# Optimization experiments

Hardware: AMD Instinct MI355X
Metric: run time of the kernel (lower is better)

The kernel has to match this reference:

```python
import jax, jax.numpy as jnp
import numpy as np

UNITS = 1024
D = 1024

def setup_inputs() -> dict:
    key = jax.random.key(0)
    ks = jax.random.split(key, 8)
    B, T = 32, 2048
    query = jax.random.normal(ks[0], (B, D), dtype=jnp.float32)
    values = jax.random.normal(ks[1], (B, T, D), dtype=jnp.float32)
    s1 = 1.0 / np.sqrt(D)
    s2 = 1.0 / np.sqrt(UNITS)
    W1 = jax.random.normal(ks[2], (D, UNITS), dtype=jnp.float32) * s1
    b1 = jnp.zeros((UNITS,), dtype=jnp.float32)
    W2 = jax.random.normal(ks[3], (D, UNITS), dtype=jnp.float32) * s1
    b2 = jnp.zeros((UNITS,), dtype=jnp.float32)
    Wv = jax.random.normal(ks[4], (UNITS, 1), dtype=jnp.float32) * s2
    bv = jnp.zeros((1,), dtype=jnp.float32)
    return {"query": query, "values": values, "W1": W1, "b1": b1,
            "W2": W2, "b2": b2, "Wv": Wv, "bv": bv}

def reference(query, values, W1, b1, W2, b2, Wv, bv):
    # query: [B, D]; values: [B, T, D]
    q_proj = query @ W1 + b1                     # [B, U]
    v_proj = jnp.einsum('btd,du->btu', values, W2) + b2  # [B, T, U]
    h = jnp.tanh(q_proj[:, None, :] + v_proj)    # [B, T, U]
    score = jnp.einsum('btu,uo->bto', h, Wv) + bv  # [B, T, 1]
    attention_weights = jax.nn.softmax(score, axis=1)  # [B, T, 1]
    context_vector = jnp.sum(attention_weights * values, axis=1)  # [B, D]
    return (context_vector, attention_weights)
```

## Files before the change

kernel.cpp:

```cpp
#include <hip/hip_runtime.h>
#include <hip/hip_bf16.h>
#include <stdint.h>


typedef unsigned short ushort_t;
typedef short bf16x8 __attribute__((ext_vector_type(8)));
typedef float f32x4 __attribute__((ext_vector_type(4)));

#define GLOBAL_AS __attribute__((address_space(1)))
#define LDS_AS    __attribute__((address_space(3)))

__device__ __forceinline__ ushort_t f2bf(float f) {
    union { float f; unsigned int u; } v;
    v.f = f;
    unsigned int u = v.u;
    unsigned int r = u + 0x7FFFu + ((u >> 16) & 1u);
    return (ushort_t)(r >> 16);
}
__device__ __forceinline__ unsigned int pk2(float a, float b) {
    union { __hip_bfloat162 h; unsigned int u; } c;
    c.h = __float22bfloat162_rn(make_float2(a, b));
    return c.u;
}
__device__ __forceinline__ float fast_tanh(float x) {
    float ax = __builtin_fabsf(x);
    float e = __expf(-2.0f * ax);
    float t = (1.0f - e) * __builtin_amdgcn_rcpf(1.0f + e);
    return __builtin_copysignf(t, x);
}

static constexpr int B_ = 32, T_ = 2048, D_ = 1024, U_ = 1024;
static constexpr int M_ = B_ * T_;
static constexpr int TRANS_B = 1024;
static constexpr int QPROJ_B = 512;
static constexpr int CONV_B  = 4096;

__global__ __launch_bounds__(256) void k_prep(const float* __restrict__ W2,
                                              const float* __restrict__ query,
                                              const float* __restrict__ W1,
                                              const float* __restrict__ b1,
                                              const float* __restrict__ b2,
                                              const float* __restrict__ values,
                                              ushort_t* __restrict__ W2T,
                                              float* __restrict__ qpb,
                                              ushort_t* __restrict__ vb) {
    __shared__ float smem[1280];
    int bid = blockIdx.x;
    const int tid = threadIdx.x;

    if (bid < TRANS_B) {
        float(*tile)[33] = (float(*)[33])smem;
        int u0 = (bid & 31) * 32, d0 = (bid >> 5) * 32;
        int tx = tid & 31, ty = tid >> 5;
#pragma unroll
        for (int r = 0; r < 4; ++r)
            tile[ty + r * 8][tx] = W2[(size_t)(d0 + ty + r * 8) * U_ + (u0 + tx)];
        __syncthreads();
#pragma unroll
        for (int r = 0; r < 4; ++r)
            W2T[(size_t)(u0 + ty + r * 8) * D_ + (d0 + tx)] = f2bf(tile[tx][ty + r * 8]);
        return;
    }
    bid -= TRANS_B;

    if (bid >= QPROJ_B) {
        const int cb = bid - QPROJ_B;
        const size_t base = (size_t)cb * 2048 + tid;
#pragma unroll
        for (int k = 0; k < 8; ++k) {
            const size_t chunk = base + (size_t)k * 256;
            const float* s = values + chunk * 8;
            f32x4 v0 = *(const f32x4*)s;
            f32x4 v1 = *(const f32x4*)(s + 4);
            uint4 p;
            p.x = pk2(v0[0], v0[1]);
            p.y = pk2(v0[2], v0[3]);
            p.z = pk2(v1[0], v1[1]);
            p.w = pk2(v1[2], v1[3]);
            *(uint4*)(vb + chunk * 8) = p;
        }
        return;
    }

    const int b = bid >> 4, uc = bid & 15;
    float* qs = smem;
    float* red = smem + 1024;
    for (int i = tid; i < D_; i += 256) qs[i] = query[b * D_ + i];
    __syncthreads();
    const int ul = tid & 63, ds = tid >> 6;
    const int u = uc * 64 + ul;
    float acc = 0.f;
#pragma unroll 8
    for (int d = ds * 256; d < ds * 256 + 256; ++d)
        acc += qs[d] * W1[(size_t)d * U_ + u];
    red[tid] = acc;
    __syncthreads();
    if (tid < 64) {
        int uu = uc * 64 + tid;
        qpb[b * U_ + uu] = red[tid] + red[tid + 64] + red[tid + 128] + red[tid + 192] +
                           b1[uu] + b2[uu];
    }
}

#define BM 128
#define BN 128
#define BK 64

template <bool ABF16>
__global__ __launch_bounds__(256) void k_score_gemm(const float* __restrict__ values,
                                                    const ushort_t* __restrict__ vb,
                                                    const ushort_t* __restrict__ W2T,
                                                    const float* __restrict__ qpb,
                                                    const float* __restrict__ Wv,
                                                    float* __restrict__ scores_partial) {
    __shared__ ushort_t As[BM * BK];
    __shared__ ushort_t Bs[BN * BK];
    __shared__ float sScore[BM];

    const int tid = threadIdx.x;
    const int lane = tid & 63;
    const int w = tid >> 6;
    const int wm = w >> 1, wn = w & 1;

    const int g = blockIdx.x;
    const int mt = ((g >> 6) << 3) | (g & 7);
    const int nt = (g >> 3) & 7;
    const int m0 = mt * BM, n0 = nt * BN;

    if (tid < BM) sScore[tid] = 0.f;

    f32x4 acc[4][4];
#pragma unroll
    for (int i = 0; i < 4; ++i)
#pragma unroll
        for (int j = 0; j < 4; ++j) acc[i][j] = (f32x4){0.f, 0.f, 0.f, 0.f};

    const int lr = lane >> 3;
    const int cB = (lane & 7) ^ lr;
    const ushort_t* bBase = W2T + (size_t)(n0 + w * 8 + lr) * D_ + cB * 8;
    const ushort_t* aBaseB = vb + (size_t)(m0 + w * 8 + lr) * D_ + cB * 8;

    const int rA = tid >> 3;
    const int cA = tid & 7;
    const int pA = cA ^ (rA & 7);
    const float* aSrc = values + (size_t)(m0 + rA) * D_ + cA * 8;
    ushort_t* aDst = As + rA * BK + pA * 8;

    const int quad = lane >> 4;
    const int l15 = lane & 15;
    const int l7 = l15 & 7;

    for (int k0 = 0; k0 < D_; k0 += BK) {
#pragma unroll
        for (int i = 0; i < 4; ++i) {
            __builtin_amdgcn_global_load_lds(
                (const GLOBAL_AS void*)(bBase + k0 + (size_t)i * 32 * D_),
                (LDS_AS void*)(Bs + i * 2048 + w * 512), 16, 0, 0);
        }
        if constexpr (ABF16) {
#pragma unroll
            for (int i = 0; i < 4; ++i) {
                __builtin_amdgcn_global_load_lds(
                    (const GLOBAL_AS void*)(aBaseB + k0 + (size_t)i * 32 * D_),
                    (LDS_AS void*)(As + i * 2048 + w * 512), 16, 0, 0);
            }
        } else {
#pragma unroll
            for (int i = 0; i < 4; ++i) {
                f32x4 v0 = *(const f32x4*)(aSrc + k0 + (size_t)i * 32 * D_);
                f32x4 v1 = *(const f32x4*)(aSrc + k0 + (size_t)i * 32 * D_ + 4);
                uint4 p;
                p.x = pk2(v0[0], v0[1]);
                p.y = pk2(v0[2], v0[3]);
                p.z = pk2(v1[0], v1[1]);
                p.w = pk2(v1[2], v1[3]);
                *(uint4*)(aDst + i * 32 * BK) = p;
            }
        }
        __syncthreads();
#pragma unroll
        for (int kk = 0; kk < BK; kk += 32) {
            bf16x8 af[4], bfr[4];
            const int cb = kk >> 3;
#pragma unroll
            for (int i = 0; i < 4; ++i) {
                int r = wm * 64 + i * 16 + l15;
                af[i] = *(const bf16x8*)(As + (r << 6) + (((quad + cb) ^ l7) << 3));
            }
#pragma unroll
            for (int j = 0; j < 4; ++j) {
                int r = wn * 64 + j * 16 + l15;
                bfr[j] = *(const bf16x8*)(Bs + (r << 6) + (((quad + cb) ^ l7) << 3));
            }
#pragma unroll
            for (int i = 0; i < 4; ++i)
#pragma unroll
                for (int j = 0; j < 4; ++j)
                    acc[i][j] = __builtin_amdgcn_mfma_f32_16x16x32_bf16(
                        af[i], bfr[j], acc[i][j], 0, 0, 0);
        }
        __syncthreads();
    }

    const int b = m0 >> 11;
    const float* qp = qpb + b * U_;
    float qv[4], wv[4];
#pragma unroll
    for (int j = 0; j < 4; ++j) {
        int u = n0 + wn * 64 + j * 16 + l15;
        qv[j] = qp[u];
        wv[j] = Wv[u];
    }
#pragma unroll
    for (int i = 0; i < 4; ++i) {
#pragma unroll
        for (int r = 0; r < 4; ++r) {
            float s = 0.f;
#pragma unroll
            for (int j = 0; j < 4; ++j) s += fast_tanh(acc[i][j][r] + qv[j]) * wv[j];
            s += __shfl_xor(s, 1);
            s += __shfl_xor(s, 2);
            s += __shfl_xor(s, 4);
            s += __shfl_xor(s, 8);
            if (l15 == 0) atomicAdd(&sScore[wm * 64 + i * 16 + quad * 4 + r], s);
        }
    }
    __syncthreads();
    if (tid < BM) scores_partial[(size_t)(m0 + tid) * 8 + nt] = sScore[tid];
}

__global__ __launch_bounds__(256) void k_softmax(const float* __restrict__ scores_partial,
                                                 const float* __restrict__ bv,
                                                 float* __restrict__ w_f,
                                                 float* __restrict__ out_w) {
    const int b = blockIdx.x;
    __shared__ float s[T_];
    __shared__ float red[4];
    const int tid = threadIdx.x;
    const float bvf = bv[0];

    float lmax = -1e30f;
    for (int t = tid; t < T_; t += 256) {
        const float* p = scores_partial + (size_t)(b * T_ + t) * 8;
        float sc = ((p[0] + p[1]) + (p[2] + p[3])) + ((p[4] + p[5]) + (p[6] + p[7])) + bvf;
        s[t] = sc;
        lmax = fmaxf(lmax, sc);
    }
    for (int off = 32; off; off >>= 1) lmax = fmaxf(lmax, __shfl_xor(lmax, off));
    if ((tid & 63) == 0) red[tid >> 6] = lmax;
    __syncthreads();
    const float gmax = fmaxf(fmaxf(red[0], red[1]), fmaxf(red[2], red[3]));

    float lsum = 0.f;
    for (int t = tid; t < T_; t += 256) {
        float e = __expf(s[t] - gmax);
        s[t] = e;
        lsum += e;
    }
    for (int off = 32; off; off >>= 1) lsum += __shfl_xor(lsum, off);
    __syncthreads();
    if ((tid & 63) == 0) red[tid >> 6] = lsum;
    __syncthreads();
    const float ginv = 1.f / ((red[0] + red[1]) + (red[2] + red[3]));

    for (int t = tid; t < T_; t += 256) {
        float wgt = s[t] * ginv;
        w_f[b * T_ + t] = wgt;
        out_w[b * T_ + t] = wgt;
    }
}

__global__ __launch_bounds__(256) void k_ctx(const float* __restrict__ values,
                                             const float* __restrict__ w_f,
                                             float* __restrict__ out_ctx) {
    const int tc = blockIdx.x;
    const int b = blockIdx.y;
    const int tid = threadIdx.x;
    __shared__ float wls[128];
    if (tid < 128) wls[tid] = w_f[b * T_ + tc * 128 + tid];
    __syncthreads();

    f32x4 acc = (f32x4){0.f, 0.f, 0.f, 0.f};
    const float* base = values + (size_t)(b * T_ + tc * 128) * D_ + tid * 4;
#pragma unroll 4
    for (int tt = 0; tt < 128; ++tt)
        acc += wls[tt] * *(const f32x4*)(base + (size_t)tt * D_);
    float* out = out_ctx + b * D_ + tid * 4;
    atomicAdd(&out[0], acc[0]);
    atomicAdd(&out[1], acc[1]);
    atomicAdd(&out[2], acc[2]);
    atomicAdd(&out[3], acc[3]);
}

extern "C" void kernel_launch(void* const* d_in, const int* in_sizes, int n_in,
                              void* d_out, int out_size, void* d_ws, size_t ws_size,
                              hipStream_t stream) {
    const float* query  = (const float*)d_in[0];
    const float* values = (const float*)d_in[1];
    const float* W1     = (const float*)d_in[2];
    const float* b1     = (const float*)d_in[3];
    const float* W2     = (const float*)d_in[4];
    const float* b2     = (const float*)d_in[5];
    const float* Wv     = (const float*)d_in[6];
    const float* bv     = (const float*)d_in[7];

    float* out_ctx = (float*)d_out;
    float* out_w   = out_ctx + B_ * D_;

    char* ws = (char*)d_ws;
    const size_t OFF_W2T = 0;
    const size_t OFF_QPB = 0x200000;
    const size_t OFF_SP  = 0x220000;
    const size_t OFF_WF  = 0x420000;
    const size_t OFF_VB  = 0x500000;
    const size_t VB_BYTES = (size_t)M_ * D_ * sizeof(ushort_t);

    ushort_t* W2T            = (ushort_t*)(ws + OFF_W2T);
    float*    qpb            = (float*)(ws + OFF_QPB);
    float*    scores_partial = (float*)(ws + OFF_SP);
    float*    w_f            = (float*)(ws + OFF_WF);
    ushort_t* vb             = (ushort_t*)(ws + OFF_VB);

    const bool use_bf16 = (ws_size >= OFF_VB + VB_BYTES);

    hipMemsetAsync(out_ctx, 0, (size_t)B_ * D_ * sizeof(float), stream);

    k_prep<<<dim3(TRANS_B + QPROJ_B + (use_bf16 ? CONV_B : 0)), 256, 0, stream>>>(
        W2, query, W1, b1, b2, values, W2T, qpb, vb);
    if (use_bf16) {
        k_score_gemm<true><<<dim3((M_ / BM) * (U_ / BN)), 256, 0, stream>>>(
            values, vb, W2T, qpb, Wv, scores_partial);
    } else {
        k_score_gemm<false><<<dim3((M_ / BM) * (U_ / BN)), 256, 0, stream>>>(
            values, vb, W2T, qpb, Wv, scores_partial);
    }
    k_softmax<<<dim3(B_), 256, 0, stream>>>(scores_partial, bv, w_f, out_w);
    k_ctx<<<dim3(16, B_), 256, 0, stream>>>(values, w_f, out_ctx);

    (void)in_sizes; (void)n_in; (void)out_size; (void)ws_size;
}
```

Measured before the change: 622.6 us.

## Drop bf16 pre-conversion pass, prefetch fp32 A tiles in registers inside GEMM

Removes the separate pass that converted the whole values tensor to bf16 in workspace. The score GEMM now reads fp32 values directly, converting in registers with a register prefetch of the next K tile overlapped with MFMA work. The q-projection is batched eight queries per block so each W1 column load is reused, and the context reduction writes partials plus a finish kernel instead of atomics and a memset. This saves roughly 400MB of conversion traffic, but the GEMM now reads twice as many A bytes per tile and keeps more registers live.

Measured after the change: 607.2 us. 2.5% less time.

```diff
diff --git a/kernel.cpp b/kernel.cpp
--- a/kernel.cpp
+++ b/kernel.cpp
@@ -32,19 +32,16 @@
 static constexpr int B_ = 32, T_ = 2048, D_ = 1024, U_ = 1024;
 static constexpr int M_ = B_ * T_;
 static constexpr int TRANS_B = 1024;
-static constexpr int QPROJ_B = 512;
-static constexpr int CONV_B  = 4096;
+static constexpr int QPROJ_B = 64;
 
 __global__ __launch_bounds__(256) void k_prep(const float* __restrict__ W2,
                                               const float* __restrict__ query,
                                               const float* __restrict__ W1,
                                               const float* __restrict__ b1,
                                               const float* __restrict__ b2,
-                                              const float* __restrict__ values,
                                               ushort_t* __restrict__ W2T,
-                                              float* __restrict__ qpb,
-                                              ushort_t* __restrict__ vb) {
-    __shared__ float smem[1280];
+                                              float* __restrict__ qpb) {
+    __shared__ float smem[8192 + 4 * 64 * 9];
     int bid = blockIdx.x;
     const int tid = threadIdx.x;
 
@@ -61,44 +58,34 @@
             W2T[(size_t)(u0 + ty + r * 8) * D_ + (d0 + tx)] = f2bf(tile[tx][ty + r * 8]);
         return;
     }
-    bid -= TRANS_B;
-
-    if (bid >= QPROJ_B) {
-        const int cb = bid - QPROJ_B;
-        const size_t base = (size_t)cb * 2048 + tid;
-#pragma unroll
-        for (int k = 0; k < 8; ++k) {
-            const size_t chunk = base + (size_t)k * 256;
-            const float* s = values + chunk * 8;
-            f32x4 v0 = *(const f32x4*)s;
-            f32x4 v1 = *(const f32x4*)(s + 4);
-            uint4 p;
-            p.x = pk2(v0[0], v0[1]);
-            p.y = pk2(v0[2], v0[3]);
-            p.z = pk2(v1[0], v1[1]);
-            p.w = pk2(v1[2], v1[3]);
-            *(uint4*)(vb + chunk * 8) = p;
-        }
-        return;
-    }
-
-    const int b = bid >> 4, uc = bid & 15;
+    const int qb = bid - TRANS_B;
+    const int bg = qb >> 4;
+    const int uc = qb & 15;
+
     float* qs = smem;
-    float* red = smem + 1024;
-    for (int i = tid; i < D_; i += 256) qs[i] = query[b * D_ + i];
-    __syncthreads();
+    float(*red)[64][9] = (float(*)[64][9])(smem + 8192);
+
+    for (int i = tid; i < 8 * 1024; i += 256)
+        qs[i] = query[(size_t)(bg * 8 + (i >> 10)) * D_ + (i & 1023)];
+    __syncthreads();
+
     const int ul = tid & 63, ds = tid >> 6;
     const int u = uc * 64 + ul;
-    float acc = 0.f;
+    float acc[8] = {0.f, 0.f, 0.f, 0.f, 0.f, 0.f, 0.f, 0.f};
 #pragma unroll 8
-    for (int d = ds * 256; d < ds * 256 + 256; ++d)
-        acc += qs[d] * W1[(size_t)d * U_ + u];
-    red[tid] = acc;
-    __syncthreads();
-    if (tid < 64) {
-        int uu = uc * 64 + tid;
-        qpb[b * U_ + uu] = red[tid] + red[tid + 64] + red[tid + 128] + red[tid + 192] +
-                           b1[uu] + b2[uu];
+    for (int d = ds * 256; d < ds * 256 + 256; ++d) {
+        const float w = W1[(size_t)d * U_ + u];
+#pragma unroll
+        for (int b = 0; b < 8; ++b) acc[b] += qs[(b << 10) + d] * w;
+    }
+#pragma unroll
+    for (int b = 0; b < 8; ++b) red[ds][ul][b] = acc[b];
+    __syncthreads();
+    for (int i = tid; i < 512; i += 256) {
+        const int b = i & 7, uu = i >> 3;
+        const float s = (red[0][uu][b] + red[1][uu][b]) + (red[2][uu][b] + red[3][uu][b]);
+        const int ug = uc * 64 + uu;
+        qpb[(size_t)(bg * 8 + b) * U_ + ug] = s + b1[ug] + b2[ug];
     }
 }
 
@@ -106,9 +93,7 @@
 #define BN 128
 #define BK 64
 
-template <bool ABF16>
 __global__ __launch_bounds__(256) void k_score_gemm(const float* __restrict__ values,
-                                                    const ushort_t* __restrict__ vb,
                                                     const ushort_t* __restrict__ W2T,
                                                     const float* __restrict__ qpb,
                                                     const float* __restrict__ Wv,
@@ -138,7 +123,6 @@
     const int lr = lane >> 3;
     const int cB = (lane & 7) ^ lr;
     const ushort_t* bBase = W2T + (size_t)(n0 + w * 8 + lr) * D_ + cB * 8;
-    const ushort_t* aBaseB = vb + (size_t)(m0 + w * 8 + lr) * D_ + cB * 8;
 
     const int rA = tid >> 3;
     const int cA = tid & 7;
@@ -150,6 +134,13 @@
     const int l15 = lane & 15;
     const int l7 = l15 & 7;
 
+    f32x4 ra0[4], ra1[4];
+#pragma unroll
+    for (int i = 0; i < 4; ++i) {
+        ra0[i] = *(const f32x4*)(aSrc + (size_t)i * 32 * D_);
+        ra1[i] = *(const f32x4*)(aSrc + (size_t)i * 32 * D_ + 4);
+    }
+
     for (int k0 = 0; k0 < D_; k0 += BK) {
 #pragma unroll
         for (int i = 0; i < 4; ++i) {
@@ -157,27 +148,23 @@
                 (const GLOBAL_AS void*)(bBase + k0 + (size_t)i * 32 * D_),
                 (LDS_AS void*)(Bs + i * 2048 + w * 512), 16, 0, 0);
         }
-        if constexpr (ABF16) {
+#pragma unroll
+        for (int i = 0; i < 4; ++i) {
+            uint4 p;
+            p.x = pk2(ra0[i][0], ra0[i][1]);
+            p.y = pk2(ra0[i][2], ra0[i][3]);
+            p.z = pk2(ra1[i][0], ra1[i][1]);
+            p.w = pk2(ra1[i][2], ra1[i][3]);
+            *(uint4*)(aDst + i * 32 * BK) = p;
+        }
+        __syncthreads();
+        if (k0 + BK < D_) {
 #pragma unroll
             for (int i = 0; i < 4; ++i) {
-                __builtin_amdgcn_global_load_lds(
-                    (const GLOBAL_AS void*)(aBaseB + k0 + (size_t)i * 32 * D_),
-                    (LDS_AS void*)(As + i * 2048 + w * 512), 16, 0, 0);
+                ra0[i] = *(const f32x4*)(aSrc + k0 + BK + (size_t)i * 32 * D_);
+                ra1[i] = *(const f32x4*)(aSrc + k0 + BK + (size_t)i * 32 * D_ + 4);
             }
-        } else {
-#pragma unroll
-            for (int i = 0; i < 4; ++i) {
-                f32x4 v0 = *(const f32x4*)(aSrc + k0 + (size_t)i * 32 * D_);
-                f32x4 v1 = *(const f32x4*)(aSrc + k0 + (size_t)i * 32 * D_ + 4);
-                uint4 p;
-                p.x = pk2(v0[0], v0[1]);
-                p.y = pk2(v0[2], v0[3]);
-                p.z = pk2(v1[0], v1[1]);
-                p.w = pk2(v1[2], v1[3]);
-                *(uint4*)(aDst + i * 32 * BK) = p;
-            }
-        }
-        __syncthreads();
+        }
 #pragma unroll
         for (int kk = 0; kk < BK; kk += 32) {
             bf16x8 af[4], bfr[4];
@@ -272,7 +259,7 @@
 
 __global__ __launch_bounds__(256) void k_ctx(const float* __restrict__ values,
                                              const float* __restrict__ w_f,
-                                             float* __restrict__ out_ctx) {
+                                             float* __restrict__ ctx_part) {
     const int tc = blockIdx.x;
     const int b = blockIdx.y;
     const int tid = threadIdx.x;
@@ -285,11 +272,18 @@
 #pragma unroll 4
     for (int tt = 0; tt < 128; ++tt)
         acc += wls[tt] * *(const f32x4*)(base + (size_t)tt * D_);
-    float* out = out_ctx + b * D_ + tid * 4;
-    atomicAdd(&out[0], acc[0]);
-    atomicAdd(&out[1], acc[1]);
-    atomicAdd(&out[2], acc[2]);
-    atomicAdd(&out[3], acc[3]);
+    *(f32x4*)(ctx_part + ((size_t)(tc * 32 + b) << 10) + tid * 4) = acc;
+}
+
+__global__ __launch_bounds__(256) void k_ctx_fin(const float* __restrict__ ctx_part,
+                                                 float* __restrict__ out_ctx) {
+    const int b = blockIdx.x;
+    const int tid = threadIdx.x;
+    f32x4 s = (f32x4){0.f, 0.f, 0.f, 0.f};
+#pragma unroll
+    for (int tc = 0; tc < 16; ++tc)
+        s += *(const f32x4*)(ctx_part + ((size_t)(tc * 32 + b) << 10) + tid * 4);
+    *(f32x4*)(out_ctx + b * D_ + tid * 4) = s;
 }
 
 extern "C" void kernel_launch(void* const* d_in, const int* in_sizes, int n_in,
@@ -312,30 +306,20 @@
     const size_t OFF_QPB = 0x200000;
     const size_t OFF_SP  = 0x220000;
     const size_t OFF_WF  = 0x420000;
-    const size_t OFF_VB  = 0x500000;
-    const size_t VB_BYTES = (size_t)M_ * D_ * sizeof(ushort_t);
+    const size_t OFF_CP  = 0x460000;
 
     ushort_t* W2T            = (ushort_t*)(ws + OFF_W2T);
     float*    qpb            = (float*)(ws + OFF_QPB);
     float*    scores_partial = (float*)(ws + OFF_SP);
     float*    w_f            = (float*)(ws + OFF_WF);
-    ushort_t* vb             = (ushort_t*)(ws + OFF_VB);
-
-    const bool use_bf16 = (ws_size >= OFF_VB + VB_BYTES);
-
-    hipMemsetAsync(out_ctx, 0, (size_t)B_ * D_ * sizeof(float), stream);
-
-    k_prep<<<dim3(TRANS_B + QPROJ_B + (use_bf16 ? CONV_B : 0)), 256, 0, stream>>>(
-        W2, query, W1, b1, b2, values, W2T, qpb, vb);
-    if (use_bf16) {
-        k_score_gemm<true><<<dim3((M_ / BM) * (U_ / BN)), 256, 0, stream>>>(
-            values, vb, W2T, qpb, Wv, scores_partial);
-    } else {
-        k_score_gemm<false><<<dim3((M_ / BM) * (U_ / BN)), 256, 0, stream>>>(
-            values, vb, W2T, qpb, Wv, scores_partial);
-    }
+    float*    ctx_part       = (float*)(ws + OFF_CP);
+
+    k_prep<<<dim3(TRANS_B + QPROJ_B), 256, 0, stream>>>(W2, query, W1, b1, b2, W2T, qpb);
+    k_score_gemm<<<dim3((M_ / BM) * (U_ / BN)), 256, 0, stream>>>(
+        values, W2T, qpb, Wv, scores_partial);
     k_softmax<<<dim3(B_), 256, 0, stream>>>(scores_partial, bv, w_f, out_w);
-    k_ctx<<<dim3(16, B_), 256, 0, stream>>>(values, w_f, out_ctx);
+    k_ctx<<<dim3(16, B_), 256, 0, stream>>>(values, w_f, ctx_part);
+    k_ctx_fin<<<dim3(B_), 256, 0, stream>>>(ctx_part, out_ctx);
 
     (void)in_sizes; (void)n_in; (void)out_size; (void)ws_size;
 }
```
